# Kernel tuning notes

Measured on AMD Instinct MI355X. Metric: run time of the kernel, lower is better.

Reference implementation:

```python
import jax, jax.numpy as jnp
import numpy as np

NUM_QUANT_BITS = 8


def setup_inputs() -> dict:
    key = jax.random.key(0)
    x = jax.random.normal(key, (64, 56, 56, 256), dtype=jnp.float32)
    return {"x": x}


def reference(x):
    # Global range (min_val/max_val default to None in the original layer)
    min_val = jnp.min(x)
    max_val = jnp.max(x)
    quantized_range = jnp.asarray(2 ** NUM_QUANT_BITS - 1, dtype=x.dtype)  # 255
    scale = quantized_range / (max_val - min_val)
    xc = jnp.clip(x, min_val, max_val)
    # round-to-nearest-even matches tf.round semantics
    out = jnp.round((xc - min_val) * scale) / scale + min_val
    return out
```

## Files before the change

kernel.cpp:

```cpp
#include <hip/hip_runtime.h>
#include <stdint.h>
#include <math.h>

typedef float vf4 __attribute__((ext_vector_type(4)));
typedef float vf2 __attribute__((ext_vector_type(2)));

__device__ __forceinline__ void mm4(vf4 v, float& mn, float& mx) {
    mn = fminf(mn, fminf(fminf(v.x, v.y), fminf(v.z, v.w)));
    mx = fmaxf(mx, fmaxf(fmaxf(v.x, v.y), fmaxf(v.z, v.w)));
}

__device__ __forceinline__ vf4 q4(vf4 v, float mn, float scale, float inv_scale) {
    vf4 r;
    r.x = rintf((v.x - mn) * scale) * inv_scale + mn;
    r.y = rintf((v.y - mn) * scale) * inv_scale + mn;
    r.z = rintf((v.z - mn) * scale) * inv_scale + mn;
    r.w = rintf((v.w - mn) * scale) * inv_scale + mn;
    return r;
}

__global__ __launch_bounds__(256) void minmax_partial(
    const float* __restrict__ x, long n,
    vf2* __restrict__ ws)
{
    const vf4* __restrict__ x4 = (const vf4*)x;
    const unsigned n4 = (unsigned)(n >> 2);

    float mn0 = INFINITY, mn1 = INFINITY, mn2 = INFINITY, mn3 = INFINITY;
    float mx0 = -INFINITY, mx1 = -INFINITY, mx2 = -INFINITY, mx3 = -INFINITY;

    const unsigned bs  = blockDim.x;
    const unsigned tid = threadIdx.x;
    const unsigned chunk = gridDim.x * bs * 4u;
    const unsigned niter = n4 / chunk;

    unsigned base = blockIdx.x * bs * 4u + tid;
    for (unsigned k = 0; k < niter; ++k, base += chunk) {
        vf4 v0 = x4[base];
        vf4 v1 = x4[base + bs];
        vf4 v2 = x4[base + 2u * bs];
        vf4 v3 = x4[base + 3u * bs];
        mm4(v0, mn0, mx0);
        mm4(v1, mn1, mx1);
        mm4(v2, mn2, mx2);
        mm4(v3, mn3, mx3);
    }
    for (unsigned idx = niter * chunk + blockIdx.x * bs + tid; idx < n4;
         idx += gridDim.x * bs)
        mm4(x4[idx], mn0, mx0);
    for (long i = (long)n4 * 4 + (long)blockIdx.x * bs + tid; i < n;
         i += (long)gridDim.x * bs) {
        float v = x[i];
        mn0 = fminf(mn0, v); mx0 = fmaxf(mx0, v);
    }

    float mn = fminf(fminf(mn0, mn1), fminf(mn2, mn3));
    float mx = fmaxf(fmaxf(mx0, mx1), fmaxf(mx2, mx3));
    #pragma unroll
    for (int off = 32; off > 0; off >>= 1) {
        mn = fminf(mn, __shfl_down(mn, off, 64));
        mx = fmaxf(mx, __shfl_down(mx, off, 64));
    }
    __shared__ float smn[4], smx[4];
    const int wave = tid >> 6;
    const int lane = tid & 63;
    if (lane == 0) { smn[wave] = mn; smx[wave] = mx; }
    __syncthreads();
    if (tid == 0) {
        vf2 p;
        p.x = fminf(fminf(smn[0], smn[1]), fminf(smn[2], smn[3]));
        p.y = fmaxf(fmaxf(smx[0], smx[1]), fmaxf(smx[2], smx[3]));
        ws[blockIdx.x] = p;
    }
}

__global__ __launch_bounds__(256) void quant_from_partials(
    const float* __restrict__ x, long n,
    float* __restrict__ o,
    const vf2* __restrict__ ws, unsigned nb)
{
    const vf4* __restrict__ x4 = (const vf4*)x;
    vf4* __restrict__ o4 = (vf4*)o;
    const unsigned n4 = (unsigned)(n >> 2);
    const unsigned bs  = blockDim.x;
    const unsigned tid = threadIdx.x;

    float mn = INFINITY, mx = -INFINITY;
    for (unsigned i = tid; i < nb; i += bs) {
        vf2 p = ws[i];
        mn = fminf(mn, p.x);
        mx = fmaxf(mx, p.y);
    }
    #pragma unroll
    for (int off = 32; off > 0; off >>= 1) {
        mn = fminf(mn, __shfl_down(mn, off, 64));
        mx = fmaxf(mx, __shfl_down(mx, off, 64));
    }
    __shared__ float smn[4], smx[4];
    const int wave = tid >> 6;
    const int lane = tid & 63;
    if (lane == 0) { smn[wave] = mn; smx[wave] = mx; }
    __syncthreads();
    const float fmn = fminf(fminf(smn[0], smn[1]), fminf(smn[2], smn[3]));
    const float fmx = fmaxf(fmaxf(smx[0], smx[1]), fmaxf(smx[2], smx[3]));
    const float scale = 255.0f / (fmx - fmn);
    const float inv_scale = 1.0f / scale;

    const unsigned chunk = gridDim.x * bs * 4u;
    const unsigned niter = n4 / chunk;
    unsigned base = blockIdx.x * bs * 4u + tid;
    for (unsigned k = 0; k < niter; ++k, base += chunk) {
        vf4 v0 = x4[base];
        vf4 v1 = x4[base + bs];
        vf4 v2 = x4[base + 2u * bs];
        vf4 v3 = x4[base + 3u * bs];
        __builtin_nontemporal_store(q4(v0, fmn, scale, inv_scale), &o4[base]);
        __builtin_nontemporal_store(q4(v1, fmn, scale, inv_scale), &o4[base + bs]);
        __builtin_nontemporal_store(q4(v2, fmn, scale, inv_scale), &o4[base + 2u * bs]);
        __builtin_nontemporal_store(q4(v3, fmn, scale, inv_scale), &o4[base + 3u * bs]);
    }
    for (unsigned idx = niter * chunk + blockIdx.x * bs + tid; idx < n4;
         idx += gridDim.x * bs)
        __builtin_nontemporal_store(q4(x4[idx], fmn, scale, inv_scale), &o4[idx]);
    for (long i = (long)n4 * 4 + (long)blockIdx.x * bs + tid; i < n;
         i += (long)gridDim.x * bs)
        o[i] = rintf((x[i] - fmn) * scale) * inv_scale + fmn;
}

extern "C" void kernel_launch(void* const* d_in, const int* in_sizes, int n_in,
                              void* d_out, int out_size, void* d_ws, size_t ws_size,
                              hipStream_t stream) {
    const float* x = (const float*)d_in[0];
    float* out = (float*)d_out;
    const long n = (long)in_sizes[0];

    const int block = 256;
    int grid = 1792;
    if (ws_size < (size_t)grid * sizeof(vf2)) {
        size_t g = ws_size / sizeof(vf2);
        grid = (g < 256) ? 256 : (int)g;
    }

    vf2* ws = (vf2*)d_ws;
    minmax_partial<<<grid, block, 0, stream>>>(x, n, ws);
    quant_from_partials<<<grid, block, 0, stream>>>(x, n, out, ws, (unsigned)grid);
}
```

Measured before the change: 366.9 us.

## Use one-tile-per-block grids and separate final min/max reduce kernel

Replaces the fixed grid-stride loops with 2048-vec4 tiles, one per block, so the grid grows to cover the whole tensor and each thread issues eight vec4 loads. Moves the reduction of per-block partials into a single-block kernel that writes the global min/max, so the quantize kernel no longer re-reduces thousands of partials in every block. The cost is an extra kernel launch and a much larger partials array, and many short-lived blocks replace the persistent ones.

```diff
diff --git a/kernel.cpp b/kernel.cpp
--- a/kernel.cpp
+++ b/kernel.cpp
@@ -19,43 +19,57 @@
     return r;
 }
 
-__global__ __launch_bounds__(256) void minmax_partial(
+#define TILE_V4 2048u
+
+__global__ __launch_bounds__(256) void minmax_partial8(
     const float* __restrict__ x, long n,
     vf2* __restrict__ ws)
 {
     const vf4* __restrict__ x4 = (const vf4*)x;
     const unsigned n4 = (unsigned)(n >> 2);
+    const unsigned tid = threadIdx.x;
 
     float mn0 = INFINITY, mn1 = INFINITY, mn2 = INFINITY, mn3 = INFINITY;
+    float mn4_ = INFINITY, mn5 = INFINITY, mn6 = INFINITY, mn7 = INFINITY;
     float mx0 = -INFINITY, mx1 = -INFINITY, mx2 = -INFINITY, mx3 = -INFINITY;
+    float mx4_ = -INFINITY, mx5 = -INFINITY, mx6 = -INFINITY, mx7 = -INFINITY;
 
-    const unsigned bs  = blockDim.x;
-    const unsigned tid = threadIdx.x;
-    const unsigned chunk = gridDim.x * bs * 4u;
-    const unsigned niter = n4 / chunk;
-
-    unsigned base = blockIdx.x * bs * 4u + tid;
-    for (unsigned k = 0; k < niter; ++k, base += chunk) {
-        vf4 v0 = x4[base];
-        vf4 v1 = x4[base + bs];
-        vf4 v2 = x4[base + 2u * bs];
-        vf4 v3 = x4[base + 3u * bs];
-        mm4(v0, mn0, mx0);
-        mm4(v1, mn1, mx1);
-        mm4(v2, mn2, mx2);
-        mm4(v3, mn3, mx3);
+    for (unsigned t = blockIdx.x; (unsigned long)t * TILE_V4 < n4; t += gridDim.x) {
+        const unsigned b0 = t * TILE_V4;
+        if (b0 + TILE_V4 <= n4) {
+            const unsigned base = b0 + tid;
+            vf4 v0 = x4[base];
+            vf4 v1 = x4[base + 256u];
+            vf4 v2 = x4[base + 512u];
+            vf4 v3 = x4[base + 768u];
+            vf4 v4 = x4[base + 1024u];
+            vf4 v5 = x4[base + 1280u];
+            vf4 v6 = x4[base + 1536u];
+            vf4 v7 = x4[base + 1792u];
+            mm4(v0, mn0, mx0);
+            mm4(v1, mn1, mx1);
+            mm4(v2, mn2, mx2);
+            mm4(v3, mn3, mx3);
+            mm4(v4, mn4_, mx4_);
+            mm4(v5, mn5, mx5);
+            mm4(v6, mn6, mx6);
+            mm4(v7, mn7, mx7);
+        } else {
+            for (unsigned idx = b0 + tid; idx < n4; idx += 256u)
+                mm4(x4[idx], mn0, mx0);
+        }
     }
-    for (unsigned idx = niter * chunk + blockIdx.x * bs + tid; idx < n4;
-         idx += gridDim.x * bs)
-        mm4(x4[idx], mn0, mx0);
-    for (long i = (long)n4 * 4 + (long)blockIdx.x * bs + tid; i < n;
-         i += (long)gridDim.x * bs) {
+    for (long i = (long)n4 * 4 + (long)blockIdx.x * 256 + tid; i < n;
+         i += (long)gridDim.x * 256)
+    {
         float v = x[i];
         mn0 = fminf(mn0, v); mx0 = fmaxf(mx0, v);
     }
 
-    float mn = fminf(fminf(mn0, mn1), fminf(mn2, mn3));
-    float mx = fmaxf(fmaxf(mx0, mx1), fmaxf(mx2, mx3));
+    float mn = fminf(fminf(fminf(mn0, mn1), fminf(mn2, mn3)),
+                     fminf(fminf(mn4_, mn5), fminf(mn6, mn7)));
+    float mx = fmaxf(fmaxf(fmaxf(mx0, mx1), fmaxf(mx2, mx3)),
+                     fmaxf(fmaxf(mx4_, mx5), fmaxf(mx6, mx7)));
     #pragma unroll
     for (int off = 32; off > 0; off >>= 1) {
         mn = fminf(mn, __shfl_down(mn, off, 64));
@@ -74,19 +88,13 @@
     }
 }
 
-__global__ __launch_bounds__(256) void quant_from_partials(
-    const float* __restrict__ x, long n,
-    float* __restrict__ o,
-    const vf2* __restrict__ ws, unsigned nb)
+__global__ __launch_bounds__(256) void reduce_partials(
+    const vf2* __restrict__ ws, unsigned nb,
+    float* __restrict__ res)
 {
-    const vf4* __restrict__ x4 = (const vf4*)x;
-    vf4* __restrict__ o4 = (vf4*)o;
-    const unsigned n4 = (unsigned)(n >> 2);
-    const unsigned bs  = blockDim.x;
     const unsigned tid = threadIdx.x;
-
     float mn = INFINITY, mx = -INFINITY;
-    for (unsigned i = tid; i < nb; i += bs) {
+    for (unsigned i = tid; i < nb; i += 256u) {
         vf2 p = ws[i];
         mn = fminf(mn, p.x);
         mx = fmaxf(mx, p.y);
@@ -101,29 +109,54 @@
     const int lane = tid & 63;
     if (lane == 0) { smn[wave] = mn; smx[wave] = mx; }
     __syncthreads();
-    const float fmn = fminf(fminf(smn[0], smn[1]), fminf(smn[2], smn[3]));
-    const float fmx = fmaxf(fmaxf(smx[0], smx[1]), fmaxf(smx[2], smx[3]));
+    if (tid == 0) {
+        res[0] = fminf(fminf(smn[0], smn[1]), fminf(smn[2], smn[3]));
+        res[1] = fmaxf(fmaxf(smx[0], smx[1]), fmaxf(smx[2], smx[3]));
+    }
+}
+
+__global__ __launch_bounds__(256) void quant8(
+    const float* __restrict__ x, long n,
+    float* __restrict__ o,
+    const float* __restrict__ res)
+{
+    const vf4* __restrict__ x4 = (const vf4*)x;
+    vf4* __restrict__ o4 = (vf4*)o;
+    const unsigned n4 = (unsigned)(n >> 2);
+    const unsigned tid = threadIdx.x;
+
+    const float fmn = res[0];
+    const float fmx = res[1];
     const float scale = 255.0f / (fmx - fmn);
     const float inv_scale = 1.0f / scale;
 
-    const unsigned chunk = gridDim.x * bs * 4u;
-    const unsigned niter = n4 / chunk;
-    unsigned base = blockIdx.x * bs * 4u + tid;
-    for (unsigned k = 0; k < niter; ++k, base += chunk) {
-        vf4 v0 = x4[base];
-        vf4 v1 = x4[base + bs];
-        vf4 v2 = x4[base + 2u * bs];
-        vf4 v3 = x4[base + 3u * bs];
-        __builtin_nontemporal_store(q4(v0, fmn, scale, inv_scale), &o4[base]);
-        __builtin_nontemporal_store(q4(v1, fmn, scale, inv_scale), &o4[base + bs]);
-        __builtin_nontemporal_store(q4(v2, fmn, scale, inv_scale), &o4[base + 2u * bs]);
-        __builtin_nontemporal_store(q4(v3, fmn, scale, inv_scale), &o4[base + 3u * bs]);
+    for (unsigned t = blockIdx.x; (unsigned long)t * TILE_V4 < n4; t += gridDim.x) {
+        const unsigned b0 = t * TILE_V4;
+        if (b0 + TILE_V4 <= n4) {
+            const unsigned base = b0 + tid;
+            vf4 v0 = x4[base];
+            vf4 v1 = x4[base + 256u];
+            vf4 v2 = x4[base + 512u];
+            vf4 v3 = x4[base + 768u];
+            vf4 v4 = x4[base + 1024u];
+            vf4 v5 = x4[base + 1280u];
+            vf4 v6 = x4[base + 1536u];
+            vf4 v7 = x4[base + 1792u];
+            __builtin_nontemporal_store(q4(v0, fmn, scale, inv_scale), &o4[base]);
+            __builtin_nontemporal_store(q4(v1, fmn, scale, inv_scale), &o4[base + 256u]);
+            __builtin_nontemporal_store(q4(v2, fmn, scale, inv_scale), &o4[base + 512u]);
+            __builtin_nontemporal_store(q4(v3, fmn, scale, inv_scale), &o4[base + 768u]);
+            __builtin_nontemporal_store(q4(v4, fmn, scale, inv_scale), &o4[base + 1024u]);
+            __builtin_nontemporal_store(q4(v5, fmn, scale, inv_scale), &o4[base + 1280u]);
+            __builtin_nontemporal_store(q4(v6, fmn, scale, inv_scale), &o4[base + 1536u]);
+            __builtin_nontemporal_store(q4(v7, fmn, scale, inv_scale), &o4[base + 1792u]);
+        } else {
+            for (unsigned idx = b0 + tid; idx < n4; idx += 256u)
+                __builtin_nontemporal_store(q4(x4[idx], fmn, scale, inv_scale), &o4[idx]);
+        }
     }
-    for (unsigned idx = niter * chunk + blockIdx.x * bs + tid; idx < n4;
-         idx += gridDim.x * bs)
-        __builtin_nontemporal_store(q4(x4[idx], fmn, scale, inv_scale), &o4[idx]);
-    for (long i = (long)n4 * 4 + (long)blockIdx.x * bs + tid; i < n;
-         i += (long)gridDim.x * bs)
+    for (long i = (long)n4 * 4 + (long)blockIdx.x * 256 + tid; i < n;
+         i += (long)gridDim.x * 256)
         o[i] = rintf((x[i] - fmn) * scale) * inv_scale + fmn;
 }
 
@@ -133,15 +166,23 @@
     const float* x = (const float*)d_in[0];
     float* out = (float*)d_out;
     const long n = (long)in_sizes[0];
+    const unsigned n4 = (unsigned)(n / 4);
 
-    const int block = 256;
-    int grid = 1792;
-    if (ws_size < (size_t)grid * sizeof(vf2)) {
-        size_t g = ws_size / sizeof(vf2);
-        grid = (g < 256) ? 256 : (int)g;
+    unsigned tiles = (n4 + TILE_V4 - 1u) / TILE_V4;
+    if (tiles == 0) tiles = 1;
+    unsigned grid = tiles;
+    const size_t need = (size_t)grid * sizeof(vf2) + 2 * sizeof(float);
+    if (ws_size < need) {
+        size_t cap = (ws_size > 2 * sizeof(float))
+                         ? (ws_size - 2 * sizeof(float)) / sizeof(vf2) : 64;
+        if (cap < 64) cap = 64;
+        if ((size_t)grid > cap) grid = (unsigned)cap;
     }
 
     vf2* ws = (vf2*)d_ws;
-    minmax_partial<<<grid, block, 0, stream>>>(x, n, ws);
-    quant_from_partials<<<grid, block, 0, stream>>>(x, n, out, ws, (unsigned)grid);
+    float* res = (float*)((char*)d_ws + (size_t)grid * sizeof(vf2));
+
+    minmax_partial8<<<grid, 256, 0, stream>>>(x, n, ws);
+    reduce_partials<<<1, 256, 0, stream>>>(ws, grid, res);
+    quant8<<<grid, 256, 0, stream>>>(x, n, out, res);
 }
```

Measured after the change: 371.7 us. Within noise of the previous version (+1.3%).
